# Kernel tuning notes

Hardware: AMD Instinct MI355X
Metric: run time of the kernel (lower is better)

The kernel has to match this reference:

```python
import jax, jax.numpy as jnp
import numpy as np

B, T, D = 8, 2048, 256
EPS_NORM = 1e-8
EPS_LN = 1e-6


def _layer_norm(x, gamma, beta):
    mu = jnp.mean(x, axis=-1, keepdims=True)
    var = jnp.var(x, axis=-1, keepdims=True)
    return (x - mu) * jax.lax.rsqrt(var + EPS_LN) * gamma + beta


def setup_inputs() -> dict:
    key = jax.random.key(0)
    ks = jax.random.split(key, 8)
    xav = np.sqrt(2.0 / (D + D)).astype(np.float32)  # xavier_uniform-ish scale
    a_fea = jax.random.normal(ks[0], (B, T, D), jnp.float32)
    v_fea = jax.random.normal(ks[1], (B, T, D), jnp.float32)
    Wv1 = jax.random.normal(ks[2], (D, D), jnp.float32) * xav
    Wv2 = jax.random.normal(ks[3], (D, D), jnp.float32) * xav
    Wa1 = jax.random.normal(ks[4], (D, D), jnp.float32) * xav
    Wa2 = jax.random.normal(ks[5], (D, D), jnp.float32) * xav
    ln_gamma = jnp.ones((D,), jnp.float32)
    ln_beta = jnp.zeros((D,), jnp.float32)
    thr_val = jnp.asarray(0.099, jnp.float32)
    return {"a_fea": a_fea, "v_fea": v_fea, "Wv1": Wv1, "Wv2": Wv2,
            "Wa1": Wa1, "Wa2": Wa2, "ln_gamma": ln_gamma, "ln_beta": ln_beta,
            "thr_val": thr_val}


def reference(a_fea, v_fea, Wv1, Wv2, Wa1, Wa2, ln_gamma, ln_beta, thr_val):
    # Dropout is identity in eval mode. Linear(bias=False): x @ W^T; here W is [in, out].
    v_b1 = jax.nn.relu(jnp.einsum('btd,dh->bth', v_fea, Wv1))
    v_b2 = jax.nn.relu(jnp.einsum('btd,dh->bth', v_fea, Wv2))
    a_b1 = jax.nn.relu(jnp.einsum('btd,dh->bth', a_fea, Wa1))
    a_b2 = jax.nn.relu(jnp.einsum('btd,dh->bth', a_fea, Wa2))

    scale = 1.0 / jnp.sqrt(jnp.asarray(v_b2.shape[2], jnp.float32))
    # relu-gated cross-modal scores [B, Tv, Ta]
    beta = jax.nn.relu(jnp.einsum('bvh,bah->bva', v_b2, a_b1) * scale)

    # v->a: normalize over audio axis, threshold-sparsify
    beta_va = beta / (jnp.sum(beta, axis=-1, keepdims=True) + EPS_NORM)
    gamma_va = jnp.where(beta_va > thr_val, beta_va, 0.0)
    # a->v: transpose of UN-normalized beta (faithful to source ordering)
    beta_av = jnp.swapaxes(beta, 1, 2)
    beta_av = beta_av / (jnp.sum(beta_av, axis=-1, keepdims=True) + EPS_NORM)
    gamma_av = jnp.where(beta_av > thr_val, beta_av, 0.0)

    a_pos = jnp.einsum('bva,bah->bvh', gamma_va, a_b2)
    v_pos = jnp.einsum('bav,bvh->bah', gamma_av, v_b1)

    v_psp = _layer_norm(v_fea + a_pos, ln_gamma, ln_beta)
    a_psp = _layer_norm(a_fea + v_pos, ln_gamma, ln_beta)
    return (v_psp + a_psp) * 0.5
```

## Files before the change

kernel.cpp:

```cpp
#include <hip/hip_runtime.h>
#include <stdint.h>

#define B_ 8
#define T_ 2048
#define D_ 256
#define M_ (B_*T_)

typedef uint16_t u16;
typedef __attribute__((ext_vector_type(8))) short   short8;
typedef __attribute__((ext_vector_type(8))) __bf16  bf16x8;
typedef __attribute__((ext_vector_type(4))) float   f32x4;

__device__ __forceinline__ float bf2f(u16 b){
    union { uint32_t u; float f; } v; v.u = ((uint32_t)b) << 16; return v.f;
}
__device__ __forceinline__ u16 f2bf(float f){
    union { float f; uint32_t u; } v; v.f = f;
    uint32_t u = v.u;
    u += 0x7FFFu + ((u >> 16) & 1u);
    return (u16)(u >> 16);
}

typedef __attribute__((address_space(1))) void gvoid;
typedef __attribute__((address_space(3))) void lvoid;
__device__ __forceinline__ void gl16(const void* g, void* l){
    __builtin_amdgcn_global_load_lds((gvoid*)(unsigned long long)g, (lvoid*)l, 16, 0, 0);
}

__global__ void k_detect(const uint32_t* g, int* flag){
    *flag = (g[0] == 0x3F803F80u) ? 0 : 1;
}

struct WtArgs { const void* w[4]; u16* wt[4]; const int* flag; };

__global__ __launch_bounds__(256) void k_wt(WtArgs a){
    int f32in = *a.flag;
    int m = blockIdx.y;
    int d = blockIdx.x;
    int h = threadIdx.x;
    float val;
    if (f32in) val = ((const float*)a.w[m])[(size_t)d * D_ + h];
    else       val = bf2f(((const u16*)a.w[m])[(size_t)d * D_ + h]);
    a.wt[m][(size_t)h * D_ + d] = f2bf(val);
}

struct ProjArgs { const void* x[4]; const u16* wt[4]; u16* y[4]; u16* yt[4]; const int* flag; };

__global__ __launch_bounds__(256) void k_proj(ProjArgs args){
    __shared__ __align__(16) u16 Xs[128][72];
    __shared__ __align__(16) u16 Ws[128][72];
    int f32in = *args.flag;
    int id = blockIdx.x;
    int m  = id & 127;
    int vh = id >> 7;
    int hh = vh & 1;
    int v  = vh >> 1;
    const u16* Wt = args.wt[v];
    u16*       Y  = args.y[v];
    u16*       YT = args.yt[v];
    int t_base = m * 128;
    int h_base = hh * 128;

    int tid  = threadIdx.x;
    int w    = tid >> 6, lane = tid & 63;
    int wm   = w >> 1, wn = w & 1;
    int l15  = lane & 15, quad = lane >> 4;

    int srow = tid >> 1;
    int shalf = tid & 1;

    f32x4 acc[4][4];
#pragma unroll
    for (int i = 0; i < 4; ++i)
#pragma unroll
        for (int j = 0; j < 4; ++j) acc[i][j] = (f32x4){0.f,0.f,0.f,0.f};

    float4 pXf[8];
    short8 pXb[4];
    short8 pW[4];

    const float* Xf = (const float*)args.x[v] + (size_t)(t_base + srow)*D_ + shalf*32;
    const u16*   Xb = (const u16*)args.x[v]   + (size_t)(t_base + srow)*D_ + shalf*32;
    const u16*   Wp = Wt + (size_t)(h_base + srow)*D_ + shalf*32;

    if (f32in){
#pragma unroll
        for (int i = 0; i < 8; ++i) pXf[i] = *(const float4*)(Xf + i*4);
    } else {
#pragma unroll
        for (int i = 0; i < 4; ++i) pXb[i] = *(const short8*)(Xb + i*8);
    }
#pragma unroll
    for (int i = 0; i < 4; ++i) pW[i] = *(const short8*)(Wp + i*8);

    for (int k0 = 0; k0 < D_; k0 += 64){
        __syncthreads();
        if (f32in){
#pragma unroll
            for (int i = 0; i < 4; ++i){
                float4 a0 = pXf[i*2], a1 = pXf[i*2+1];
                short8 o;
                o[0]=(short)f2bf(a0.x); o[1]=(short)f2bf(a0.y); o[2]=(short)f2bf(a0.z); o[3]=(short)f2bf(a0.w);
                o[4]=(short)f2bf(a1.x); o[5]=(short)f2bf(a1.y); o[6]=(short)f2bf(a1.z); o[7]=(short)f2bf(a1.w);
                *(short8*)(&Xs[srow][shalf*32 + i*8]) = o;
            }
        } else {
#pragma unroll
            for (int i = 0; i < 4; ++i) *(short8*)(&Xs[srow][shalf*32 + i*8]) = pXb[i];
        }
#pragma unroll
        for (int i = 0; i < 4; ++i) *(short8*)(&Ws[srow][shalf*32 + i*8]) = pW[i];

        int kn = k0 + 64;
        if (kn < D_){
            if (f32in){
#pragma unroll
                for (int i = 0; i < 8; ++i) pXf[i] = *(const float4*)(Xf + kn + i*4);
            } else {
#pragma unroll
                for (int i = 0; i < 4; ++i) pXb[i] = *(const short8*)(Xb + kn + i*8);
            }
#pragma unroll
            for (int i = 0; i < 4; ++i) pW[i] = *(const short8*)(Wp + kn + i*8);
        }
        __syncthreads();

#pragma unroll
        for (int kc = 0; kc < 2; ++kc){
            bf16x8 af[4], bf[4];
#pragma unroll
            for (int i = 0; i < 4; ++i){
                af[i] = __builtin_bit_cast(bf16x8,
                         *(const short8*)(&Xs[wm*64 + i*16 + l15][kc*32 + quad*8]));
                bf[i] = __builtin_bit_cast(bf16x8,
                         *(const short8*)(&Ws[wn*64 + i*16 + l15][kc*32 + quad*8]));
            }
#pragma unroll
            for (int mt = 0; mt < 4; ++mt)
#pragma unroll
                for (int nt = 0; nt < 4; ++nt)
                    acc[mt][nt] = __builtin_amdgcn_mfma_f32_16x16x32_bf16(
                                      af[mt], bf[nt], acc[mt][nt], 0, 0, 0);
        }
    }

    int v0 = t_base + wm*64;
    int h0 = h_base + wn*64;
#pragma unroll
    for (int mt = 0; mt < 4; ++mt){
#pragma unroll
        for (int nt = 0; nt < 4; ++nt){
            int col = h0 + nt*16 + l15;
            u16 q[4];
#pragma unroll
            for (int r = 0; r < 4; ++r){
                float s = acc[mt][nt][r]; s = s > 0.f ? s : 0.f;
                q[r] = f2bf(s);
            }
            if (Y){
#pragma unroll
                for (int r = 0; r < 4; ++r)
                    Y[(size_t)(v0 + mt*16 + quad*4 + r)*D_ + col] = q[r];
            }
            if (YT){
                int row0 = v0 + mt*16 + quad*4;
                int bb   = row0 >> 11;
                int tl   = row0 & (T_-1);
                uint2 pk;
                pk.x = (uint32_t)q[0] | ((uint32_t)q[1] << 16);
                pk.y = (uint32_t)q[2] | ((uint32_t)q[3] << 16);
                *(uint2*)(YT + ((size_t)(bb*D_ + col))*T_ + tl) = pk;
            }
        }
    }
}

__global__ __launch_bounds__(256) void k_score(const u16* vb2, const u16* ab1,
                                               u16* beta, u16* betaT,
                                               float* rowsum, float* colsum){
    __shared__ __align__(16) u16 As[128][72];
    __shared__ __align__(16) u16 Bs[128][72];
    int id = blockIdx.x;
    int b  = id & 7;
    int t  = id >> 3;
    int mb = t & 15;
    int ab = t >> 4;
    int tid  = threadIdx.x;
    int w    = tid >> 6, lane = tid & 63;
    int wm   = w >> 1, wn = w & 1;
    int l15  = lane & 15, quad = lane >> 4;
    int v_base = mb*128;
    int a_base = ab*128;

    const u16* vb = vb2 + (size_t)b*T_*D_;
    const u16* an = ab1 + (size_t)b*T_*D_;
    u16*   bbp = beta  + (size_t)b*T_*T_;
    u16*   bbt = betaT + (size_t)b*T_*T_;
    float* rs  = rowsum + b*T_;
    float* cs  = colsum + b*T_;

    int kk = tid & 7;
    int mm = tid >> 3;

    f32x4 acc[4][4];
#pragma unroll
    for (int i = 0; i < 4; ++i)
#pragma unroll
        for (int j = 0; j < 4; ++j) acc[i][j] = (f32x4){0.f,0.f,0.f,0.f};

    short8 pA[4], pB[4];
#pragma unroll
    for (int i = 0; i < 4; ++i){
        int row = mm + i*32;
        pA[i] = *(const short8*)(vb + (size_t)(v_base + row)*D_ + kk*8);
        pB[i] = *(const short8*)(an + (size_t)(a_base + row)*D_ + kk*8);
    }

    for (int k0 = 0; k0 < D_; k0 += 64){
        __syncthreads();
#pragma unroll
        for (int i = 0; i < 4; ++i){
            int row = mm + i*32;
            *(short8*)(&As[row][kk*8]) = pA[i];
            *(short8*)(&Bs[row][kk*8]) = pB[i];
        }
        int kn = k0 + 64;
        if (kn < D_){
#pragma unroll
            for (int i = 0; i < 4; ++i){
                int row = mm + i*32;
                pA[i] = *(const short8*)(vb + (size_t)(v_base + row)*D_ + kn + kk*8);
                pB[i] = *(const short8*)(an + (size_t)(a_base + row)*D_ + kn + kk*8);
            }
        }
        __syncthreads();

#pragma unroll
        for (int kc = 0; kc < 2; ++kc){
            bf16x8 af[4], bf[4];
#pragma unroll
            for (int i = 0; i < 4; ++i){
                af[i] = __builtin_bit_cast(bf16x8,
                         *(const short8*)(&As[wm*64 + i*16 + l15][kc*32 + quad*8]));
                bf[i] = __builtin_bit_cast(bf16x8,
                         *(const short8*)(&Bs[wn*64 + i*16 + l15][kc*32 + quad*8]));
            }
#pragma unroll
            for (int mt = 0; mt < 4; ++mt)
#pragma unroll
                for (int nt = 0; nt < 4; ++nt)
                    acc[mt][nt] = __builtin_amdgcn_mfma_f32_16x16x32_bf16(
                                      af[mt], bf[nt], acc[mt][nt], 0, 0, 0);
        }
    }

    int v0 = v_base + wm*64;
    int a0 = a_base + wn*64;
    float rsum[4][4];
    float csum[4] = {0.f,0.f,0.f,0.f};
#pragma unroll
    for (int mt = 0; mt < 4; ++mt)
#pragma unroll
        for (int r = 0; r < 4; ++r) rsum[mt][r] = 0.f;

#pragma unroll
    for (int mt = 0; mt < 4; ++mt){
#pragma unroll
        for (int nt = 0; nt < 4; ++nt){
            u16 q[4];
#pragma unroll
            for (int r = 0; r < 4; ++r){
                float s = acc[mt][nt][r] * 0.0625f;
                s = s > 0.f ? s : 0.f;
                q[r] = f2bf(s);
                bbp[(size_t)(v0 + mt*16 + quad*4 + r)*T_ + a0 + nt*16 + l15] = q[r];
                rsum[mt][r] += s;
                csum[nt]    += s;
            }
            uint2 pk;
            pk.x = (uint32_t)q[0] | ((uint32_t)q[1] << 16);
            pk.y = (uint32_t)q[2] | ((uint32_t)q[3] << 16);
            *(uint2*)(bbt + (size_t)(a0 + nt*16 + l15)*T_ + v0 + mt*16 + quad*4) = pk;
        }
    }
#pragma unroll
    for (int mt = 0; mt < 4; ++mt){
#pragma unroll
        for (int r = 0; r < 4; ++r){
            float v = rsum[mt][r];
            v += __shfl_xor(v, 1);
            v += __shfl_xor(v, 2);
            v += __shfl_xor(v, 4);
            v += __shfl_xor(v, 8);
            if (l15 == 0) atomicAdd(&rs[v0 + mt*16 + quad*4 + r], v);
        }
    }
#pragma unroll
    for (int nt = 0; nt < 4; ++nt){
        float v = csum[nt];
        v += __shfl_xor(v, 16);
        v += __shfl_xor(v, 32);
        if (quad == 0) atomicAdd(&cs[a0 + nt*16 + l15], v);
    }
}

__global__ __launch_bounds__(256) void k_pos3(const u16* beta, const u16* betaT,
                                              const u16* ab2T, const u16* vb1T,
                                              const float* rowsum, const float* colsum,
                                              const void* thrp, const int* flag,
                                              u16* apos, u16* vpos){
    __shared__ __align__(16) u16 SL[2][2][128*64];
    int f32in = *flag;
    int id = blockIdx.x;
    int nb    = id & 1;
    int mb    = (id >> 1) & 15;
    int b     = (id >> 5) & 7;
    int which = id >> 8;

    const u16* A   = (which ? betaT : beta) + (size_t)b*T_*T_;
    const u16* Bt  = (which ? vb1T  : ab2T) + (size_t)b*T_*D_;
    const float* nrm = (which ? colsum : rowsum) + b*T_;
    u16* outb = (which ? vpos : apos) + (size_t)b*T_*D_;

    float thr = f32in ? *(const float*)thrp : bf2f(*(const u16*)thrp);

    int tid = threadIdx.x;
    int w = tid >> 6, lane = tid & 63;
    int wm = w >> 1, wn = w & 1;
    int l15 = lane & 15, quad = lane >> 4;

    int m0 = mb * 128;
    int h0 = nb * 128;

    int srow = w*32 + (lane >> 3);
    int schk = (lane & 7) ^ ((lane >> 3) & 7);
    const u16* gA = A  + (size_t)(m0 + srow)*T_ + schk*8;
    const u16* gB = Bt + (size_t)(h0 + srow)*T_ + schk*8;

    float thra[4];
#pragma unroll
    for (int i = 0; i < 4; ++i)
        thra[i] = thr * (nrm[m0 + wm*64 + i*16 + l15] + 1e-8f);

    f32x4 acc[4][4];
#pragma unroll
    for (int i = 0; i < 4; ++i)
#pragma unroll
        for (int j = 0; j < 4; ++j) acc[i][j] = (f32x4){0.f,0.f,0.f,0.f};

#pragma unroll
    for (int c = 0; c < 4; ++c){
        gl16(gA + (size_t)c*8*T_, &SL[0][0][(w*32 + c*8)*64]);
        gl16(gB + (size_t)c*8*T_, &SL[0][1][(w*32 + c*8)*64]);
    }

    int q = 0;
    for (int k0 = 0; k0 < T_; k0 += 64){
        __syncthreads();
        int kn = k0 + 64;
        if (kn < T_){
#pragma unroll
            for (int c = 0; c < 4; ++c){
                gl16(gA + (size_t)c*8*T_ + kn, &SL[q^1][0][(w*32 + c*8)*64]);
                gl16(gB + (size_t)c*8*T_ + kn, &SL[q^1][1][(w*32 + c*8)*64]);
            }
        }
        const u16* Asb = &SL[q][0][0];
        const u16* Bsb = &SL[q][1][0];
#pragma unroll
        for (int kc = 0; kc < 2; ++kc){
            int sw = ((kc*4 + quad) ^ (l15 & 7)) * 8;
            bf16x8 af[4], bfr[4];
#pragma unroll
            for (int i = 0; i < 4; ++i){
                short8 ra = *(const short8*)(Asb + (size_t)(wm*64 + i*16 + l15)*64 + sw);
                short8 o;
#pragma unroll
                for (int j = 0; j < 8; ++j){
                    u16 e = (u16)(short)ra[j];
                    o[j] = (bf2f(e) > thra[i]) ? ra[j] : (short)0;
                }
                af[i]  = __builtin_bit_cast(bf16x8, o);
                bfr[i] = __builtin_bit_cast(bf16x8,
                          *(const short8*)(Bsb + (size_t)(wn*64 + i*16 + l15)*64 + sw));
            }
#pragma unroll
            for (int mt = 0; mt < 4; ++mt)
#pragma unroll
                for (int nt = 0; nt < 4; ++nt)
                    acc[mt][nt] = __builtin_amdgcn_mfma_f32_16x16x32_bf16(
                                      af[mt], bfr[nt], acc[mt][nt], 0, 0, 0);
        }
        q ^= 1;
    }

#pragma unroll
    for (int mt = 0; mt < 4; ++mt){
#pragma unroll
        for (int r = 0; r < 4; ++r){
            int row = m0 + wm*64 + mt*16 + quad*4 + r;
            float iv = 1.f / (nrm[row] + 1e-8f);
#pragma unroll
            for (int nt = 0; nt < 4; ++nt)
                outb[(size_t)row*D_ + h0 + wn*64 + nt*16 + l15] =
                    f2bf(acc[mt][nt][r] * iv);
        }
    }
}

__global__ __launch_bounds__(256) void k_ln(const void* vfea, const void* afea,
                                            const u16* apos, const u16* vpos,
                                            const void* g, const void* lnb,
                                            const int* flag, void* out){
    int f32in = *flag;
    int row = blockIdx.x;
    int c   = threadIdx.x;
    size_t idx = (size_t)row * D_ + c;
    float xv = f32in ? ((const float*)vfea)[idx] : bf2f(((const u16*)vfea)[idx]);
    float xa = f32in ? ((const float*)afea)[idx] : bf2f(((const u16*)afea)[idx]);
    float x1 = xv + bf2f(apos[idx]);
    float x2 = xa + bf2f(vpos[idx]);
    float s1 = x1, q1 = x1*x1, s2 = x2, q2 = x2*x2;
#pragma unroll
    for (int off = 1; off < 64; off <<= 1){
        s1 += __shfl_xor(s1, off);
        q1 += __shfl_xor(q1, off);
        s2 += __shfl_xor(s2, off);
        q2 += __shfl_xor(q2, off);
    }
    __shared__ float red[4][4];
    int wave = threadIdx.x >> 6;
    if ((threadIdx.x & 63) == 0){
        red[0][wave] = s1; red[1][wave] = q1; red[2][wave] = s2; red[3][wave] = q2;
    }
    __syncthreads();
    s1 = red[0][0]+red[0][1]+red[0][2]+red[0][3];
    q1 = red[1][0]+red[1][1]+red[1][2]+red[1][3];
    s2 = red[2][0]+red[2][1]+red[2][2]+red[2][3];
    q2 = red[3][0]+red[3][1]+red[3][2]+red[3][3];
    const float invD = 1.f / (float)D_;
    float mu1 = s1*invD, mu2 = s2*invD;
    float var1 = q1*invD - mu1*mu1;
    float var2 = q2*invD - mu2*mu2;
    float rs1 = rsqrtf(var1 + 1e-6f);
    float rs2 = rsqrtf(var2 + 1e-6f);
    float gg = f32in ? ((const float*)g)[c]   : bf2f(((const u16*)g)[c]);
    float bv = f32in ? ((const float*)lnb)[c] : bf2f(((const u16*)lnb)[c]);
    float y = 0.5f * (((x1-mu1)*rs1)*gg + bv + ((x2-mu2)*rs2)*gg + bv);
    if (f32in) ((float*)out)[idx] = y;
    else       ((u16*)out)[idx]   = f2bf(y);
}

extern "C" void kernel_launch(void* const* d_in, const int* in_sizes, int n_in,
                              void* d_out, int out_size, void* d_ws, size_t ws_size,
                              hipStream_t stream){
    (void)in_sizes; (void)n_in; (void)out_size; (void)ws_size;
    const void* a_fea = d_in[0];
    const void* v_fea = d_in[1];
    const void* Wv1   = d_in[2];
    const void* Wv2   = d_in[3];
    const void* Wa1   = d_in[4];
    const void* Wa2   = d_in[5];
    const void* lng   = d_in[6];
    const void* lnb   = d_in[7];
    const void* thrp  = d_in[8];
    char* ws = (char*)d_ws;

    const size_t ACT  = (size_t)M_ * D_ * 2;
    const size_t BETA = (size_t)B_ * T_ * T_ * 2;
    size_t off_wt    = 0;
    size_t off_vb2   = 524288;
    size_t off_ab1   = off_vb2  + ACT;
    size_t off_vb1T  = off_ab1  + ACT;
    size_t off_ab2T  = off_vb1T + ACT;
    size_t off_beta  = off_ab2T + ACT;
    size_t off_betaT = off_beta  + BETA;
    size_t off_rsum  = off_betaT + BETA;
    size_t off_csum  = off_rsum + (size_t)B_*T_*4;
    size_t off_apos  = off_csum + (size_t)B_*T_*4;
    size_t off_vpos  = off_apos + ACT;
    size_t off_flag  = off_vpos + ACT;

    u16* wt0   = (u16*)(ws + off_wt);
    u16* vb2   = (u16*)(ws + off_vb2);
    u16* ab1   = (u16*)(ws + off_ab1);
    u16* vb1T  = (u16*)(ws + off_vb1T);
    u16* ab2T  = (u16*)(ws + off_ab2T);
    u16* beta  = (u16*)(ws + off_beta);
    u16* betaT = (u16*)(ws + off_betaT);
    float* rowsum = (float*)(ws + off_rsum);
    float* colsum = (float*)(ws + off_csum);
    u16*   apos   = (u16*)(ws + off_apos);
    u16*   vpos   = (u16*)(ws + off_vpos);
    int*   flag   = (int*)(ws + off_flag);

    hipMemsetAsync(ws + off_rsum, 0, 2 * (size_t)B_ * T_ * sizeof(float), stream);

    k_detect<<<1, 1, 0, stream>>>((const uint32_t*)lng, flag);

    WtArgs wa;
    wa.w[0] = Wv1; wa.w[1] = Wv2; wa.w[2] = Wa1; wa.w[3] = Wa2;
    for (int i = 0; i < 4; ++i) wa.wt[i] = wt0 + (size_t)i * D_ * D_;
    wa.flag = flag;
    k_wt<<<dim3(256,4), 256, 0, stream>>>(wa);

    ProjArgs pa;
    pa.x[0] = v_fea; pa.x[1] = v_fea; pa.x[2] = a_fea; pa.x[3] = a_fea;
    for (int i = 0; i < 4; ++i) pa.wt[i] = wa.wt[i];
    pa.y[0] = nullptr; pa.y[1] = vb2; pa.y[2] = ab1; pa.y[3] = nullptr;
    pa.yt[0] = vb1T;   pa.yt[1] = nullptr; pa.yt[2] = nullptr; pa.yt[3] = ab2T;
    pa.flag = flag;
    k_proj<<<4*2*(M_/128), 256, 0, stream>>>(pa);

    k_score<<<8*16*16, 256, 0, stream>>>(vb2, ab1, beta, betaT, rowsum, colsum);

    k_pos3<<<512, 256, 0, stream>>>(beta, betaT, ab2T, vb1T, rowsum, colsum,
                                    thrp, flag, apos, vpos);

    k_ln<<<M_, 256, 0, stream>>>(v_fea, a_fea, apos, vpos, lng, lnb, flag, d_out);
}
```

Before: 251.3 us.

## Retile pos GEMM warps to 32x128 and use packed-u16 threshold masking

Reorganizes the sparse gating GEMM so each wave owns 32 rows by the full 128 output columns instead of a 64x64 quadrant. This halves per-wave threshold masking of the beta fragments, at the cost of loading more B fragments from LDS. The per-element float compare-and-select is replaced by packed 16-bit subtract and arithmetic shift to build masks two elements at a time. This relies on beta being non-negative bf16 and truncates the threshold to bf16.

Result: no change. 247.9 us (-1.3%).

```diff
diff --git a/kernel.cpp b/kernel.cpp
--- a/kernel.cpp
+++ b/kernel.cpp
@@ -10,6 +10,7 @@
 typedef __attribute__((ext_vector_type(8))) short   short8;
 typedef __attribute__((ext_vector_type(8))) __bf16  bf16x8;
 typedef __attribute__((ext_vector_type(4))) float   f32x4;
+typedef __attribute__((ext_vector_type(4))) uint32_t u32x4;
 
 __device__ __forceinline__ float bf2f(u16 b){
     union { uint32_t u; float f; } v; v.u = ((uint32_t)b) << 16; return v.f;
@@ -304,7 +305,7 @@
     }
 }
 
-__global__ __launch_bounds__(256) void k_pos3(const u16* beta, const u16* betaT,
+__global__ __launch_bounds__(256) void k_pos4(const u16* beta, const u16* betaT,
                                               const u16* ab2T, const u16* vb1T,
                                               const float* rowsum, const float* colsum,
                                               const void* thrp, const int* flag,
@@ -326,7 +327,6 @@
 
     int tid = threadIdx.x;
     int w = tid >> 6, lane = tid & 63;
-    int wm = w >> 1, wn = w & 1;
     int l15 = lane & 15, quad = lane >> 4;
 
     int m0 = mb * 128;
@@ -337,16 +337,20 @@
     const u16* gA = A  + (size_t)(m0 + srow)*T_ + schk*8;
     const u16* gB = Bt + (size_t)(h0 + srow)*T_ + schk*8;
 
-    float thra[4];
-#pragma unroll
-    for (int i = 0; i < 4; ++i)
-        thra[i] = thr * (nrm[m0 + wm*64 + i*16 + l15] + 1e-8f);
-
-    f32x4 acc[4][4];
-#pragma unroll
-    for (int i = 0; i < 4; ++i)
-#pragma unroll
-        for (int j = 0; j < 4; ++j) acc[i][j] = (f32x4){0.f,0.f,0.f,0.f};
+    uint32_t thp[2];
+#pragma unroll
+    for (int i = 0; i < 2; ++i){
+        float ts = thr * (nrm[m0 + w*32 + i*16 + l15] + 1e-8f);
+        union { float f; uint32_t u; } cv; cv.f = ts;
+        uint32_t th16 = cv.u >> 16;
+        thp[i] = th16 * 0x10001u;
+    }
+
+    f32x4 acc[2][8];
+#pragma unroll
+    for (int i = 0; i < 2; ++i)
+#pragma unroll
+        for (int j = 0; j < 8; ++j) acc[i][j] = (f32x4){0.f,0.f,0.f,0.f};
 
 #pragma unroll
     for (int c = 0; c < 4; ++c){
@@ -370,40 +374,43 @@
 #pragma unroll
         for (int kc = 0; kc < 2; ++kc){
             int sw = ((kc*4 + quad) ^ (l15 & 7)) * 8;
-            bf16x8 af[4], bfr[4];
-#pragma unroll
-            for (int i = 0; i < 4; ++i){
-                short8 ra = *(const short8*)(Asb + (size_t)(wm*64 + i*16 + l15)*64 + sw);
-                short8 o;
-#pragma unroll
-                for (int j = 0; j < 8; ++j){
-                    u16 e = (u16)(short)ra[j];
-                    o[j] = (bf2f(e) > thra[i]) ? ra[j] : (short)0;
+            bf16x8 af[2];
+#pragma unroll
+            for (int i = 0; i < 2; ++i){
+                u32x4 ra = *(const u32x4*)(Asb + (size_t)(w*32 + i*16 + l15)*64 + sw);
+                u32x4 om;
+#pragma unroll
+                for (int jd = 0; jd < 4; ++jd){
+                    uint32_t t, m;
+                    asm("v_pk_sub_u16 %0, %1, %2" : "=v"(t) : "v"(thp[i]), "v"(ra[jd]));
+                    asm("v_pk_ashrrev_i16 %0, 15, %1" : "=v"(m) : "v"(t));
+                    om[jd] = ra[jd] & m;
                 }
-                af[i]  = __builtin_bit_cast(bf16x8, o);
-                bfr[i] = __builtin_bit_cast(bf16x8,
-                          *(const short8*)(Bsb + (size_t)(wn*64 + i*16 + l15)*64 + sw));
-            }
-#pragma unroll
-            for (int mt = 0; mt < 4; ++mt)
-#pragma unroll
-                for (int nt = 0; nt < 4; ++nt)
-                    acc[mt][nt] = __builtin_amdgcn_mfma_f32_16x16x32_bf16(
-                                      af[mt], bfr[nt], acc[mt][nt], 0, 0, 0);
+                af[i] = __builtin_bit_cast(bf16x8, om);
+            }
+#pragma unroll
+            for (int nt = 0; nt < 8; ++nt){
+                bf16x8 bfr = __builtin_bit_cast(bf16x8,
+                              *(const short8*)(Bsb + (size_t)(nt*16 + l15)*64 + sw));
+                acc[0][nt] = __builtin_amdgcn_mfma_f32_16x16x32_bf16(
+                                  af[0], bfr, acc[0][nt], 0, 0, 0);
+                acc[1][nt] = __builtin_amdgcn_mfma_f32_16x16x32_bf16(
+                                  af[1], bfr, acc[1][nt], 0, 0, 0);
+            }
         }
         q ^= 1;
     }
 
 #pragma unroll
-    for (int mt = 0; mt < 4; ++mt){
+    for (int i = 0; i < 2; ++i){
 #pragma unroll
         for (int r = 0; r < 4; ++r){
-            int row = m0 + wm*64 + mt*16 + quad*4 + r;
+            int row = m0 + w*32 + i*16 + quad*4 + r;
             float iv = 1.f / (nrm[row] + 1e-8f);
 #pragma unroll
-            for (int nt = 0; nt < 4; ++nt)
-                outb[(size_t)row*D_ + h0 + wn*64 + nt*16 + l15] =
-                    f2bf(acc[mt][nt][r] * iv);
+            for (int nt = 0; nt < 8; ++nt)
+                outb[(size_t)row*D_ + h0 + nt*16 + l15] =
+                    f2bf(acc[i][nt][r] * iv);
         }
     }
 }
@@ -514,7 +521,7 @@
 
     k_score<<<8*16*16, 256, 0, stream>>>(vb2, ab1, beta, betaT, rowsum, colsum);
 
-    k_pos3<<<512, 256, 0, stream>>>(beta, betaT, ab2T, vb1T, rowsum, colsum,
+    k_pos4<<<512, 256, 0, stream>>>(beta, betaT, ab2T, vb1T, rowsum, colsum,
                                     thrp, flag, apos, vpos);
 
     k_ln<<<M_, 256, 0, stream>>>(v_fea, a_fea, apos, vpos, lng, lnb, flag, d_out);
```
